# Performance work log

Hardware: AMD Instinct MI355X
Metric: run time of the kernel (lower is better)

The kernel has to match this reference:

```python
import jax, jax.numpy as jnp
import numpy as np

SOS_TOKEN = 0
EOS_TOKEN = 29
B, S, ENC = 128, 400, 512   # batch, encoder max seq len, encoder feature dim
E, H, D, P, V = 256, 512, 128, 128, 30  # embed, dec hidden, dec out, attn proj, vocab
T = 600  # inference timesteps


def setup_inputs() -> dict:
    key = jax.random.key(0)
    ks = jax.random.split(key, 20)
    u = lambda k, sh: jax.random.uniform(k, sh, jnp.float32, -0.1, 0.1)
    n = lambda k, sh, s=0.02: s * jax.random.normal(k, sh, jnp.float32)
    embed = n(ks[0], (V, E), 1.0).at[EOS_TOKEN].set(0.0)  # padding_idx=EOS
    inp = dict(
        encoder_outputs=jax.random.normal(ks[1], (B, S, ENC), jnp.float32),
        encoder_lens=jax.random.randint(ks[2], (B,), S // 2, S + 1),
        embed=embed,
        W_ih1=u(ks[3], (4 * H, E + P)), W_hh1=u(ks[4], (4 * H, H)),
        b_ih1=u(ks[5], (4 * H,)), b_hh1=u(ks[6], (4 * H,)),
        W_ih2=u(ks[7], (4 * D, H)), W_hh2=u(ks[8], (4 * D, D)),
        b_ih2=u(ks[9], (4 * D,)), b_hh2=u(ks[10], (4 * D,)),
        Wk=n(ks[11], (P, ENC)), bk=jnp.zeros((P,), jnp.float32),
        Wv=n(ks[12], (P, ENC)), bv=jnp.zeros((P,), jnp.float32),
        Wq=n(ks[13], (P, D)), bq=jnp.zeros((P,), jnp.float32),
        b_char=jnp.zeros((V,), jnp.float32),
    )
    return inp


def _lstm_cell(x, h, c, W_ih, W_hh, b_ih, b_hh):
    gates = x @ W_ih.T + h @ W_hh.T + b_ih + b_hh
    i, f, g, o = jnp.split(gates, 4, axis=-1)
    c2 = jax.nn.sigmoid(f) * c + jax.nn.sigmoid(i) * jnp.tanh(g)
    return jax.nn.sigmoid(o) * jnp.tanh(c2), c2


def reference(encoder_outputs, encoder_lens, embed,
              W_ih1, W_hh1, b_ih1, b_hh1,
              W_ih2, W_hh2, b_ih2, b_hh2,
              Wk, bk, Wv, bv, Wq, bq, b_char):
    # precompute attention keys/values and mask (set_key_value_mask)
    keyv = encoder_outputs @ Wk.T + bk           # [B, S, P]
    valv = encoder_outputs @ Wv.T + bv           # [B, S, P]
    mask = jnp.arange(S)[None, :] < encoder_lens[:, None]  # [B, S]
    scale = 1.0 / np.sqrt(P).astype(np.float32)

    char0 = jnp.full((B,), SOS_TOKEN, jnp.int32)
    h1 = jnp.zeros((B, H), jnp.float32); c1 = jnp.zeros((B, H), jnp.float32)
    h2 = jnp.zeros((B, D), jnp.float32); c2 = jnp.zeros((B, D), jnp.float32)
    ctx0 = jnp.zeros((B, P), jnp.float32)

    def step(carry, _):
        char, h1, c1, h2, c2, ctx = carry
        ce = embed[char]                                   # [B, E]
        x = jnp.concatenate([ce, ctx], axis=1)
        h1n, c1n = _lstm_cell(x, h1, c1, W_ih1, W_hh1, b_ih1, b_hh1)
        h2n, c2n = _lstm_cell(h1n, h2, c2, W_ih2, W_hh2, b_ih2, b_hh2)
        q = h2n @ Wq.T + bq                                # [B, P] (attention.query)
        e = jnp.einsum('bsp,bp->bs', keyv, q) * scale
        w = jax.nn.softmax(jnp.where(mask, e, -1e9), axis=-1)
        ctxn = jnp.einsum('bs,bsp->bp', w, valv)           # [B, P]
        out_emb = jnp.concatenate([q, ctxn], axis=1)       # [B, P+P] == [B, E]
        pred = out_emb @ embed.T + b_char                  # tied char_prob weight
        charn = jnp.argmax(pred, axis=1).astype(jnp.int32)
        return (charn, h1n, c1n, h2n, c2n, ctxn), (pred, w[0])

    _, (preds, attn0) = jax.lax.scan(step, (char0, h1, c1, h2, c2, ctx0), None, length=T)
    predictions = jnp.transpose(preds, (1, 0, 2))  # [B, T, V]
    attention_plot = attn0                          # [T, S]
    return predictions, attention_plot
```

## Files before the change

kernel.cpp:

```cpp
#include <hip/hip_runtime.h>
#include <math.h>

#define B_   128
#define S_   400
#define ENC_ 512
#define E_   256
#define H_   512
#define D_   128
#define P_   128
#define V_   30
#define T_   600

#define KEYV_OFF 0
#define VALV_OFF (KEYV_OFF + B_*S_*P_)
#define H1_OFF   (VALV_OFF + B_*S_*P_)
#define H2T_OFF  (H1_OFF + 2*H_*B_)
#define H2R_OFF  (H2T_OFF + 2*D_*B_)
#define CTXT_OFF (H2R_OFF + B_*D_)
#define CHR_OFF  (CTXT_OFF + P_*B_)
#define WS_FLOATS (CHR_OFF + B_)

#define PRED_N (B_*T_*V_)
#define NBLK 256
#define NTHR 512

#define W1_BASE 0
#define W2_BASE 14336
#define SCR     24576
#define LDS_FLOATS (SCR + 13120)

__device__ __forceinline__ float sigm_(float x){ return 1.0f/(1.0f + expf(-x)); }

__device__ __forceinline__ float ldA(const float* p){
  return __hip_atomic_load(p, __ATOMIC_RELAXED, __HIP_MEMORY_SCOPE_AGENT);
}
__device__ __forceinline__ void stA(float* p, float v){
  __hip_atomic_store(p, v, __ATOMIC_RELAXED, __HIP_MEMORY_SCOPE_AGENT);
}
__device__ __forceinline__ int ldAi(const int* p){
  return __hip_atomic_load(p, __ATOMIC_RELAXED, __HIP_MEMORY_SCOPE_AGENT);
}
__device__ __forceinline__ void stAi(int* p, int v){
  __hip_atomic_store(p, v, __ATOMIC_RELAXED, __HIP_MEMORY_SCOPE_AGENT);
}
__device__ __forceinline__ void ldA2f(const float* p, float& a, float& b){
  unsigned long long v = __hip_atomic_load((const unsigned long long*)p,
                         __ATOMIC_RELAXED, __HIP_MEMORY_SCOPE_AGENT);
  a = __uint_as_float((unsigned)v);
  b = __uint_as_float((unsigned)(v>>32));
}

__device__ __forceinline__ void gbar(int* bar){
  asm volatile("s_waitcnt vmcnt(0)" ::: "memory");
  __syncthreads();
  if (threadIdx.x == 0){
    const int g0 = __hip_atomic_load(bar, __ATOMIC_RELAXED, __HIP_MEMORY_SCOPE_AGENT);
    asm volatile("" ::: "memory");
    int* leaf = bar + 64 + (blockIdx.x & 7)*32;
    int lo = __hip_atomic_fetch_add(leaf, 1, __ATOMIC_RELAXED, __HIP_MEMORY_SCOPE_AGENT);
    bool done = false;
    if (lo == 31){
      int ro = __hip_atomic_fetch_add(bar+32, 1, __ATOMIC_RELAXED, __HIP_MEMORY_SCOPE_AGENT);
      if (ro == 7){
        #pragma unroll
        for (int i=0;i<8;++i)
          __hip_atomic_store(bar+64+i*32, 0, __ATOMIC_RELAXED, __HIP_MEMORY_SCOPE_AGENT);
        __hip_atomic_store(bar+32, 0, __ATOMIC_RELAXED, __HIP_MEMORY_SCOPE_AGENT);
        asm volatile("s_waitcnt vmcnt(0)" ::: "memory");
        __hip_atomic_fetch_add(bar, 1, __ATOMIC_RELAXED, __HIP_MEMORY_SCOPE_AGENT);
        done = true;
      }
    }
    if (!done){
      while (__hip_atomic_load(bar, __ATOMIC_RELAXED, __HIP_MEMORY_SCOPE_AGENT) == g0)
        __builtin_amdgcn_s_sleep(4);
    }
  }
  __syncthreads();
}

__global__ __launch_bounds__(256) void k_kv(const float* __restrict__ enc,
    const float* __restrict__ Wk, const float* __restrict__ bk,
    const float* __restrict__ Wv, const float* __restrict__ bv,
    float* __restrict__ ws)
{
  __shared__ float As[32][68];
  __shared__ float Bs[32][68];
  const int tid = threadIdx.x;
  const int tx = tid & 15, ty = tid >> 4;
  const int n0 = blockIdx.x * 64;
  const int c0 = blockIdx.y * 64;
  float acc[4][4] = {};
  for (int k0 = 0; k0 < ENC_; k0 += 32){
    #pragma unroll
    for (int i = 0; i < 8; ++i){
      int idx = tid + 256*i;
      int kk = idx & 31, nl = idx >> 5;
      As[kk][nl] = enc[(size_t)(n0+nl)*ENC_ + k0 + kk];
    }
    #pragma unroll
    for (int i = 0; i < 8; ++i){
      int idx = tid + 256*i;
      int kk = idx & 31, cl = idx >> 5;
      int c = c0 + cl; int p = c & 127;
      const float* W = (c < 128) ? Wk : Wv;
      Bs[kk][cl] = W[(size_t)p*ENC_ + k0 + kk];
    }
    __syncthreads();
    #pragma unroll
    for (int kk = 0; kk < 32; ++kk){
      float4 a4 = *(const float4*)&As[kk][ty*4];
      float4 b4 = *(const float4*)&Bs[kk][tx*4];
      float aa[4] = {a4.x, a4.y, a4.z, a4.w};
      float bb[4] = {b4.x, b4.y, b4.z, b4.w};
      #pragma unroll
      for (int i=0;i<4;++i)
        #pragma unroll
        for (int j=0;j<4;++j) acc[i][j] += aa[i]*bb[j];
    }
    __syncthreads();
  }
  float* keyv = ws + KEYV_OFF;
  float* valv = ws + VALV_OFF;
  #pragma unroll
  for (int i=0;i<4;++i){
    int n = n0 + ty*4 + i; int b = n / S_; int s = n - b*S_;
    #pragma unroll
    for (int j=0;j<4;++j){
      int c = c0 + tx*4 + j;
      float v = acc[i][j];
      if (c < 128) keyv[((size_t)b*S_+s)*P_ + c]       = v + bk[c];
      else         valv[((size_t)b*S_+s)*P_ + (c-128)] = v + bv[c-128];
    }
  }
}

__global__ __launch_bounds__(NTHR, 1) void k_persist(
    const float* __restrict__ embed,
    const float* __restrict__ Wih1, const float* __restrict__ Whh1,
    const float* __restrict__ bih1, const float* __restrict__ bhh1,
    const float* __restrict__ Wih2, const float* __restrict__ Whh2,
    const float* __restrict__ bih2, const float* __restrict__ bhh2,
    const float* __restrict__ Wq, const float* __restrict__ bq,
    const float* __restrict__ bchar, const int* __restrict__ lens,
    float* ws, float* out)
{
  extern __shared__ float smem[];
  const int tid = threadIdx.x;
  const int bid = blockIdx.x;
  int* bar = (int*)(ws + WS_FLOATS);

  float* ctxT = ws + CTXT_OFF;
  int*   chrg = (int*)(ws + CHR_OFF);
  float* h2R  = ws + H2R_OFF;

  float* Wl  = smem + W1_BASE;
  float* W2l = smem + W2_BASE;
  float* scr = smem + SCR;

  const int lane = tid & 63;
  const int so8  = tid >> 6;

  const int ib = bid & 1, ug = bid >> 1, b0 = ib*64;
  const int iq = lane & 15, rq = lane >> 4;
  const int u1 = tid >> 6;
  const int J1 = ug*4 + (u1 & 3);
  const int sA  = (tid & 31)*2;
  const int kbA = tid >> 5;

  const int ig2 = bid & 3, ug2 = bid >> 2, b02 = ig2*32;
  const int iq2 = lane & 7, rq2 = lane >> 3;
  const int u2 = tid >> 5;
  const int J2 = ug2*4 + (u2 & 3);
  const int sB  = (tid & 15)*2;
  const int kbB = tid >> 4;

  const int it3 = bid & 127;
  const float* keyv3 = ws + KEYV_OFF + (size_t)it3*S_*P_;
  const float* valv3 = ws + VALV_OFF + (size_t)it3*S_*P_;
  const int lenb = lens[it3];
  const float bqr  = bq[tid >> 2];
  const float bchr = ((tid >> 4) < V_) ? bchar[tid >> 4] : 0.f;
  float* qs3   = scr;
  float* es3   = scr + 128;
  float* hs3   = scr + 528;
  float* redw3 = scr + 656;
  float* red33 = scr + 672;
  float* oes3  = scr + 2784;
  float* pred3 = scr + 3040;

  {
    const int r = tid & 15, kb = tid >> 4;
    const int R = (r >> 2)*H_ + ug*4 + (r & 3);
    for (int j = 0; j < 28; ++j){
      int k = kb*28 + j;
      float v = (k < 384) ? Wih1[(size_t)R*384 + k] : Whh1[(size_t)R*H_ + (k-384)];
      Wl[k*16 + r] = v;
    }
  }
  if (bid < 128){
    const int r = tid & 15, kb = tid >> 4;
    const int R = (r >> 2)*D_ + ug2*4 + (r & 3);
    for (int j = 0; j < 20; ++j){
      int k = kb*20 + j;
      float v = (k < 512) ? Wih2[(size_t)R*H_ + k] : Whh2[(size_t)R*D_ + (k-512)];
      W2l[k*16 + r] = v;
    }
  }
  __syncthreads();

  float c1r = 0.f, c2r = 0.f;
  float b1s[4], b2s[4];
  #pragma unroll
  for (int g=0; g<4; ++g){
    b1s[g] = bih1[g*H_ + J1] + bhh1[g*H_ + J1];
    b2s[g] = (bid < 128) ? (bih2[g*D_ + J2] + bhh2[g*D_ + J2]) : 0.f;
  }

  for (int t = 0; t < T_; ++t){
    {
      const float* h1oT = ws + H1_OFF + (size_t)(t&1)*H_*B_;
      float*       h1nT = ws + H1_OFF + (size_t)((t+1)&1)*H_*B_;
      float* Xs  = scr;
      float* red = scr + 4096;
      int*   schs= (int*)(scr + 12800);

      if (tid < 64) schs[tid] = ldAi(chrg + b0 + tid);
      __syncthreads();
      const int chA = schs[sA], chB = schs[sA+1];

      float xr[4][8];
      auto LOADX = [&](int p, float* dst){
        if (p < 4){
          const float4 va = *(const float4*)(embed + (size_t)chA*E_ + p*64 + kbA*4);
          const float4 vb = *(const float4*)(embed + (size_t)chB*E_ + p*64 + kbA*4);
          dst[0]=va.x; dst[1]=vb.x; dst[2]=va.y; dst[3]=vb.y;
          dst[4]=va.z; dst[5]=vb.z; dst[6]=va.w; dst[7]=vb.w;
        } else {
          const float* base = (p < 6) ? (ctxT + (size_t)(p*64-256)*B_)
                                      : (h1oT + (size_t)(p*64-384)*B_);
          #pragma unroll
          for (int j=0;j<4;++j)
            ldA2f(base + (size_t)(kbA*4+j)*B_ + b0 + sA, dst[j*2], dst[j*2+1]);
        }
      };
      LOADX(0,xr[0]); LOADX(1,xr[1]); LOADX(2,xr[2]); LOADX(3,xr[3]);

      float acc[4][4] = {};
      for (int p = 0; p < 14; ++p){
        float* xc = xr[p&3];
        #pragma unroll
        for (int j=0;j<4;++j){
          const int kl = kbA*4 + j;
          *(float2*)&Xs[kl*64 + (((sA>>2)+kl)&15)*4 + (sA&3)]
            = make_float2(xc[j*2], xc[j*2+1]);
        }
        __syncthreads();
        if (p + 4 < 14) LOADX(p + 4, xr[p&3]);
        float4 xv[8], wv[8];
        #pragma unroll
        for (int it = 0; it < 8; ++it){
          const int kl = so8*8 + it;
          xv[it] = *(const float4*)&Xs[kl*64 + ((iq + kl)&15)*4];
          wv[it] = *(const float4*)&Wl[(p*64 + kl)*16 + rq*4];
        }
        #pragma unroll
        for (int it = 0; it < 8; ++it){
          float xa[4] = {xv[it].x, xv[it].y, xv[it].z, xv[it].w};
          float wa[4] = {wv[it].x, wv[it].y, wv[it].z, wv[it].w};
          #pragma unroll
          for (int i=0;i<4;++i)
            #pragma unroll
            for (int j=0;j<4;++j) acc[i][j] += xa[i]*wa[j];
        }
        __syncthreads();
      }
      #pragma unroll
      for (int j=0;j<4;++j)
        *(float4*)&red[so8*1088 + (rq*4+j)*68 + iq*4]
          = make_float4(acc[0][j], acc[1][j], acc[2][j], acc[3][j]);
      __syncthreads();
      if (tid < 256){
        const int item = tid & 63;
        float gate[4];
        #pragma unroll
        for (int g=0; g<4; ++g){
          float s = 0.f;
          #pragma unroll
          for (int w=0; w<8; ++w) s += red[w*1088 + (g*4+(u1&3))*68 + item];
          gate[g] = s + b1s[g];
        }
        float cn = sigm_(gate[1])*c1r + sigm_(gate[0])*tanhf(gate[2]);
        float hn = sigm_(gate[3])*tanhf(cn);
        c1r = cn;
        stA(h1nT + (size_t)J1*B_ + b0 + item, hn);
      }
    }
    gbar(bar);

    if (bid < 128){
      const float* h1nT = ws + H1_OFF + (size_t)((t+1)&1)*H_*B_;
      const float* h2oT = ws + H2T_OFF + (size_t)(t&1)*D_*B_;
      float*       h2nT = ws + H2T_OFF + (size_t)((t+1)&1)*D_*B_;
      float* Xs2  = scr;
      float* red2 = scr + 2048;

      float xr2[4][4];
      auto LOADX2 = [&](int p, float* dst){
        const float* base = (p < 8) ? (h1nT + (size_t)(p*64)*B_)
                                    : (h2oT + (size_t)(p*64-512)*B_);
        #pragma unroll
        for (int j=0;j<2;++j)
          ldA2f(base + (size_t)(kbB*2+j)*B_ + b02 + sB, dst[j*2], dst[j*2+1]);
      };
      LOADX2(0,xr2[0]); LOADX2(1,xr2[1]); LOADX2(2,xr2[2]); LOADX2(3,xr2[3]);

      float acc2[4][2] = {};
      for (int p = 0; p < 10; ++p){
        float* xc = xr2[p&3];
        #pragma unroll
        for (int j=0;j<2;++j){
          const int kl = kbB*2 + j;
          *(float2*)&Xs2[kl*32 + (((sB>>2)+kl)&7)*4 + (sB&3)]
            = make_float2(xc[j*2], xc[j*2+1]);
        }
        __syncthreads();
        if (p + 4 < 10) LOADX2(p + 4, xr2[p&3]);
        float4 xv2[8]; float2 wv2[8];
        #pragma unroll
        for (int it = 0; it < 8; ++it){
          const int kl = so8*8 + it;
          xv2[it] = *(const float4*)&Xs2[kl*32 + ((iq2 + kl)&7)*4];
          wv2[it] = *(const float2*)&W2l[(p*64 + kl)*16 + rq2*2];
        }
        #pragma unroll
        for (int it = 0; it < 8; ++it){
          float xa[4] = {xv2[it].x, xv2[it].y, xv2[it].z, xv2[it].w};
          #pragma unroll
          for (int i=0;i<4;++i){
            acc2[i][0] += xa[i]*wv2[it].x;
            acc2[i][1] += xa[i]*wv2[it].y;
          }
        }
        __syncthreads();
      }
      #pragma unroll
      for (int j=0;j<2;++j)
        *(float4*)&red2[so8*576 + (rq2*2+j)*36 + iq2*4]
          = make_float4(acc2[0][j], acc2[1][j], acc2[2][j], acc2[3][j]);
      __syncthreads();
      if (tid < 128){
        const int item = tid & 31;
        float gate[4];
        #pragma unroll
        for (int g=0; g<4; ++g){
          float s = 0.f;
          #pragma unroll
          for (int w=0; w<8; ++w) s += red2[w*576 + (g*4+(u2&3))*36 + item];
          gate[g] = s + b2s[g];
        }
        float cn = sigm_(gate[1])*c2r + sigm_(gate[0])*tanhf(gate[2]);
        float hn = sigm_(gate[3])*tanhf(cn);
        c2r = cn;
        stA(h2nT + (size_t)J2*B_ + b02 + item, hn);
        stA(h2R  + (size_t)(b02+item)*D_ + J2, hn);
      }
    } else {
      float wacc = 0.f;
      const float4* kp = (const float4*)keyv3;
      #pragma unroll
      for (int j = 0; j < 8; ++j){
        float4 v = kp[tid + j*512];
        wacc += v.x + v.y + v.z + v.w;
      }
      asm volatile("" :: "v"(wacc));
    }
    gbar(bar);

    if (bid >= 128){
      if (tid < 128) hs3[tid] = ldA(h2R + (size_t)it3*D_ + tid);
      __syncthreads();
      {
        const int r = tid >> 2, kq = tid & 3;
        const float* wr = Wq + (size_t)r*D_ + kq*32;
        float a = 0.f;
        #pragma unroll
        for (int j=0;j<8;++j){
          float4 wvq = *(const float4*)(wr + j*4);
          float4 hv = *(const float4*)&hs3[kq*32 + j*4];
          a += wvq.x*hv.x + wvq.y*hv.y + wvq.z*hv.z + wvq.w*hv.w;
        }
        a += __shfl_down(a, 2, 4);
        a += __shfl_down(a, 1, 4);
        if (kq == 0) qs3[r] = a + bqr;
      }
      __syncthreads();
      float sv = -INFINITY;
      if (tid < lenb){
        const float4* kr = (const float4*)(keyv3 + (size_t)tid*P_);
        float a = 0.f;
        #pragma unroll 8
        for (int d=0; d<32; ++d){
          float4 kv = kr[d];
          float4 qv = *(const float4*)&qs3[d*4];
          a += kv.x*qv.x + kv.y*qv.y + kv.z*qv.z + kv.w*qv.w;
        }
        sv = a * 0.08838834764831845f;
      }
      float mv = sv;
      #pragma unroll
      for (int o=32; o; o>>=1) mv = fmaxf(mv, __shfl_xor(mv, o));
      if ((tid & 63) == 0) redw3[tid >> 6] = mv;
      __syncthreads();
      const float m = fmaxf(fmaxf(fmaxf(redw3[0],redw3[1]),fmaxf(redw3[2],redw3[3])),
                            fmaxf(fmaxf(redw3[4],redw3[5]),fmaxf(redw3[6],redw3[7])));
      float pv = 0.f;
      if (tid < lenb){ pv = expf(sv - m); es3[tid] = pv; }
      float sm = pv;
      #pragma unroll
      for (int o=32; o; o>>=1) sm += __shfl_xor(sm, o);
      if ((tid & 63) == 0) redw3[8 + (tid >> 6)] = sm;
      __syncthreads();
      const float sum = ((redw3[8]+redw3[9])+(redw3[10]+redw3[11]))
                      + ((redw3[12]+redw3[13])+(redw3[14]+redw3[15]));
      {
        const int p4 = tid & 31, sg = tid >> 5;
        float a0=0,a1=0,a2=0,a3=0;
        const int rend = min(sg*25 + 25, lenb);
        #pragma unroll 4
        for (int r = sg*25; r < rend; ++r){
          float e = es3[r];
          float4 v = *(const float4*)(valv3 + (size_t)r*P_ + p4*4);
          a0 += e*v.x; a1 += e*v.y; a2 += e*v.z; a3 += e*v.w;
        }
        *(float4*)&red33[sg*132 + p4*4] = make_float4(a0,a1,a2,a3);
      }
      __syncthreads();
      if (tid < 128){
        float c = 0.f;
        #pragma unroll
        for (int sg=0; sg<16; ++sg) c += red33[sg*132 + tid];
        c /= sum;
        stA(ctxT + (size_t)tid*B_ + it3, c);
        oes3[tid] = qs3[tid]; oes3[128+tid] = c;
      }
      __syncthreads();
      {
        const int v = tid >> 4, k16 = tid & 15;
        float a = 0.f;
        if (v < V_){
          const float4* er = (const float4*)(embed + (size_t)v*E_ + k16*16);
          #pragma unroll
          for (int j=0;j<4;++j){
            float4 ev = er[j];
            float4 ov = *(const float4*)&oes3[k16*16 + j*4];
            a += ev.x*ov.x + ev.y*ov.y + ev.z*ov.z + ev.w*ov.w;
          }
        }
        a += __shfl_down(a, 8, 16);
        a += __shfl_down(a, 4, 16);
        a += __shfl_down(a, 2, 16);
        a += __shfl_down(a, 1, 16);
        if (v < V_ && k16 == 0){
          float pvv = a + bchr;
          pred3[v] = pvv;
          out[((size_t)it3*T_ + t)*V_ + v] = pvv;
        }
      }
      __syncthreads();
      if (tid < 32){
        float val = (tid < V_) ? pred3[tid] : -INFINITY;
        int idx = tid;
        #pragma unroll
        for (int o = 16; o > 0; o >>= 1){
          float ov = __shfl_down(val, o, 32);
          int oi = __shfl_down(idx, o, 32);
          if (ov > val || (ov == val && oi < idx)){ val = ov; idx = oi; }
        }
        if (tid == 0) stAi(chrg + it3, idx);
      }
      if (it3 == 0 && tid < S_)
        out[PRED_N + (size_t)t*S_ + tid] = (tid < lenb) ? es3[tid]/sum : 0.f;
    }
    gbar(bar);
  }
}

extern "C" void kernel_launch(void* const* d_in, const int* in_sizes, int n_in,
                              void* d_out, int out_size, void* d_ws, size_t ws_size,
                              hipStream_t stream)
{
  (void)in_sizes; (void)n_in; (void)out_size; (void)ws_size;
  const float* enc   = (const float*)d_in[0];
  const int*   lens  = (const int*)d_in[1];
  const float* embed = (const float*)d_in[2];
  const float* Wih1  = (const float*)d_in[3];
  const float* Whh1  = (const float*)d_in[4];
  const float* bih1  = (const float*)d_in[5];
  const float* bhh1  = (const float*)d_in[6];
  const float* Wih2  = (const float*)d_in[7];
  const float* Whh2  = (const float*)d_in[8];
  const float* bih2  = (const float*)d_in[9];
  const float* bhh2  = (const float*)d_in[10];
  const float* Wk    = (const float*)d_in[11];
  const float* bk    = (const float*)d_in[12];
  const float* Wv    = (const float*)d_in[13];
  const float* bv    = (const float*)d_in[14];
  const float* Wq    = (const float*)d_in[15];
  const float* bq    = (const float*)d_in[16];
  const float* bchar = (const float*)d_in[17];
  float* out = (float*)d_out;
  float* ws  = (float*)d_ws;

  hipMemsetAsync((char*)d_ws + (size_t)H1_OFF*sizeof(float), 0,
                 (size_t)(WS_FLOATS - H1_OFF)*sizeof(float) + 2048, stream);
  hipLaunchKernelGGL(k_kv, dim3(800,4), dim3(256), 0, stream, enc, Wk, bk, Wv, bv, ws);

  hipFuncSetAttribute((const void*)k_persist,
                      hipFuncAttributeMaxDynamicSharedMemorySize, LDS_FLOATS*4);
  hipLaunchKernelGGL(k_persist, dim3(NBLK), dim3(NTHR), LDS_FLOATS*4, stream,
                     embed, Wih1, Whh1, bih1, bhh1,
                     Wih2, Whh2, bih2, bhh2,
                     Wq, bq, bchar, lens, ws, out);
}
```

Before: 25.77 ms.

## Split attention across two blocks per batch row and defer combine into next step

The attention phase now runs on all 256 blocks: each batch row's sequence is split into two halves of up to 200 positions. Each half computes partial max, sum and weighted values, and the second block merges them with a log-sum-exp combine. The combine, projection and argmax are deferred into the start of the next timestep. The LSTM1 matmul is reordered so the h1 panels are computed first, and a counter spin-wait holds off the embedding and context panels until the combine has published the new chars and context. This doubles attention parallelism and overlaps the output head with LSTM1 work, at the cost of extra workspace traffic and an extra fine-grained sync.

Result: slower. 61.84 ms (+139.9%).

```diff
diff --git a/kernel.cpp b/kernel.cpp
--- a/kernel.cpp
+++ b/kernel.cpp
@@ -18,7 +18,10 @@
 #define H2R_OFF  (H2T_OFF + 2*D_*B_)
 #define CTXT_OFF (H2R_OFF + B_*D_)
 #define CHR_OFF  (CTXT_OFF + P_*B_)
-#define WS_FLOATS (CHR_OFF + B_)
+#define PV0_OFF  (CHR_OFF + B_)
+#define MS0_OFF  (PV0_OFF + B_*P_)
+#define ES0_OFF  (MS0_OFF + 2*B_)
+#define WS_FLOATS (ES0_OFF + 200)
 
 #define PRED_N (B_*T_*V_)
 #define NBLK 256
@@ -27,7 +30,7 @@
 #define W1_BASE 0
 #define W2_BASE 14336
 #define SCR     24576
-#define LDS_FLOATS (SCR + 13120)
+#define LDS_FLOATS (SCR + 13312)
 
 __device__ __forceinline__ float sigm_(float x){ return 1.0f/(1.0f + expf(-x)); }
 
@@ -148,15 +151,22 @@
   extern __shared__ float smem[];
   const int tid = threadIdx.x;
   const int bid = blockIdx.x;
-  int* bar = (int*)(ws + WS_FLOATS);
+  int* bar  = (int*)(ws + WS_FLOATS);
+  int* cnt2 = bar + 512;
 
   float* ctxT = ws + CTXT_OFF;
   int*   chrg = (int*)(ws + CHR_OFF);
   float* h2R  = ws + H2R_OFF;
+  float* pv0g = ws + PV0_OFF;
+  float* ms0g = ws + MS0_OFF;
+  float* es0g = ws + ES0_OFF;
 
   float* Wl  = smem + W1_BASE;
   float* W2l = smem + W2_BASE;
   float* scr = smem + SCR;
+  float* qs3k   = scr + 12864;
+  float* oesA   = scr + 12992;
+  float* pred3A = scr + 13248;
 
   const int lane = tid & 63;
   const int so8  = tid >> 6;
@@ -175,19 +185,15 @@
   const int sB  = (tid & 15)*2;
   const int kbB = tid >> 4;
 
+  const int h3  = bid >> 7;
   const int it3 = bid & 127;
   const float* keyv3 = ws + KEYV_OFF + (size_t)it3*S_*P_;
   const float* valv3 = ws + VALV_OFF + (size_t)it3*S_*P_;
   const int lenb = lens[it3];
+  const int cw  = h3 ? (lenb - 200) : 200;
+  const int s0w = h3*200;
   const float bqr  = bq[tid >> 2];
   const float bchr = ((tid >> 4) < V_) ? bchar[tid >> 4] : 0.f;
-  float* qs3   = scr;
-  float* es3   = scr + 128;
-  float* hs3   = scr + 528;
-  float* redw3 = scr + 656;
-  float* red33 = scr + 672;
-  float* oes3  = scr + 2784;
-  float* pred3 = scr + 3040;
 
   {
     const int r = tid & 15, kb = tid >> 4;
@@ -217,6 +223,59 @@
     b2s[g] = (bid < 128) ? (bih2[g*D_ + J2] + bhh2[g*D_ + J2]) : 0.f;
   }
 
+  float mhK = -INFINITY, smK = 0.f, pvcK = 0.f, esK = 0.f;
+
+  auto COMBINE = [&](int tp){
+    const float m0 = ldA(ms0g + it3*2), s0v = ldA(ms0g + it3*2 + 1);
+    const float m  = fmaxf(m0, mhK);
+    const float e0 = expf(m0 - m), e1 = expf(mhK - m);
+    const float sum = s0v*e0 + smK*e1;
+    if (tid < 128){
+      float c = (ldA(pv0g + (size_t)it3*P_ + tid)*e0 + pvcK*e1) / sum;
+      stA(ctxT + (size_t)tid*B_ + it3, c);
+      oesA[tid] = qs3k[tid]; oesA[128+tid] = c;
+    }
+    __syncthreads();
+    {
+      const int v = tid >> 4, k16 = tid & 15;
+      float a = 0.f;
+      if (v < V_){
+        const float4* er = (const float4*)(embed + (size_t)v*E_ + k16*16);
+        #pragma unroll
+        for (int j=0;j<4;++j){
+          float4 ev = er[j];
+          float4 ov = *(const float4*)&oesA[k16*16 + j*4];
+          a += ev.x*ov.x + ev.y*ov.y + ev.z*ov.z + ev.w*ov.w;
+        }
+      }
+      a += __shfl_down(a, 8, 16);
+      a += __shfl_down(a, 4, 16);
+      a += __shfl_down(a, 2, 16);
+      a += __shfl_down(a, 1, 16);
+      if (v < V_ && k16 == 0){
+        float pvv = a + bchr;
+        pred3A[v] = pvv;
+        out[((size_t)it3*T_ + tp)*V_ + v] = pvv;
+      }
+    }
+    __syncthreads();
+    if (tid < 32){
+      float val = (tid < V_) ? pred3A[tid] : -INFINITY;
+      int idx = tid;
+      #pragma unroll
+      for (int o = 16; o > 0; o >>= 1){
+        float ov = __shfl_down(val, o, 32);
+        int oi = __shfl_down(idx, o, 32);
+        if (ov > val || (ov == val && oi < idx)){ val = ov; idx = oi; }
+      }
+      if (tid == 0) stAi(chrg + it3, idx);
+    }
+    if (it3 == 0 && tid < S_){
+      float v = (tid < 200) ? ldA(es0g + tid)*e0 : esK*e1;
+      out[PRED_N + (size_t)tp*S_ + tid] = v / sum;
+    }
+  };
+
   for (int t = 0; t < T_; ++t){
     {
       const float* h1oT = ws + H1_OFF + (size_t)(t&1)*H_*B_;
@@ -225,38 +284,36 @@
       float* red = scr + 4096;
       int*   schs= (int*)(scr + 12800);
 
-      if (tid < 64) schs[tid] = ldAi(chrg + b0 + tid);
-      __syncthreads();
-      const int chA = schs[sA], chB = schs[sA+1];
+      if (bid >= 128 && t > 0){
+        COMBINE(t-1);
+        asm volatile("s_waitcnt vmcnt(0)" ::: "memory");
+        __syncthreads();
+        if (tid == 0)
+          (void)__hip_atomic_fetch_add(cnt2, 1, __ATOMIC_RELAXED, __HIP_MEMORY_SCOPE_AGENT);
+      }
 
       float xr[4][8];
-      auto LOADX = [&](int p, float* dst){
-        if (p < 4){
-          const float4 va = *(const float4*)(embed + (size_t)chA*E_ + p*64 + kbA*4);
-          const float4 vb = *(const float4*)(embed + (size_t)chB*E_ + p*64 + kbA*4);
-          dst[0]=va.x; dst[1]=vb.x; dst[2]=va.y; dst[3]=vb.y;
-          dst[4]=va.z; dst[5]=vb.z; dst[6]=va.w; dst[7]=vb.w;
-        } else {
-          const float* base = (p < 6) ? (ctxT + (size_t)(p*64-256)*B_)
-                                      : (h1oT + (size_t)(p*64-384)*B_);
-          #pragma unroll
-          for (int j=0;j<4;++j)
-            ldA2f(base + (size_t)(kbA*4+j)*B_ + b0 + sA, dst[j*2], dst[j*2+1]);
-        }
+      float acc[4][4] = {};
+      int chA = 0, chB = 0;
+      auto LOADH = [&](int p, float* dst){
+        const float* base = h1oT + (size_t)(p*64-384)*B_;
+        #pragma unroll
+        for (int j=0;j<4;++j)
+          ldA2f(base + (size_t)(kbA*4+j)*B_ + b0 + sA, dst[j*2], dst[j*2+1]);
       };
-      LOADX(0,xr[0]); LOADX(1,xr[1]); LOADX(2,xr[2]); LOADX(3,xr[3]);
-
-      float acc[4][4] = {};
-      for (int p = 0; p < 14; ++p){
-        float* xc = xr[p&3];
-        #pragma unroll
-        for (int j=0;j<4;++j){
-          const int kl = kbA*4 + j;
-          *(float2*)&Xs[kl*64 + (((sA>>2)+kl)&15)*4 + (sA&3)]
-            = make_float2(xc[j*2], xc[j*2+1]);
-        }
-        __syncthreads();
-        if (p + 4 < 14) LOADX(p + 4, xr[p&3]);
+      auto LOADE = [&](int p, float* dst){
+        const float4 va = *(const float4*)(embed + (size_t)chA*E_ + p*64 + kbA*4);
+        const float4 vb = *(const float4*)(embed + (size_t)chB*E_ + p*64 + kbA*4);
+        dst[0]=va.x; dst[1]=vb.x; dst[2]=va.y; dst[3]=vb.y;
+        dst[4]=va.z; dst[5]=vb.z; dst[6]=va.w; dst[7]=vb.w;
+      };
+      auto LOADC = [&](int p, float* dst){
+        const float* base = ctxT + (size_t)(p*64-256)*B_;
+        #pragma unroll
+        for (int j=0;j<4;++j)
+          ldA2f(base + (size_t)(kbA*4+j)*B_ + b0 + sA, dst[j*2], dst[j*2+1]);
+      };
+      auto PANEL = [&](int p){
         float4 xv[8], wv[8];
         #pragma unroll
         for (int it = 0; it < 8; ++it){
@@ -273,6 +330,40 @@
             #pragma unroll
             for (int j=0;j<4;++j) acc[i][j] += xa[i]*wa[j];
         }
+      };
+      auto STORE = [&](float* xc){
+        #pragma unroll
+        for (int j=0;j<4;++j){
+          const int kl = kbA*4 + j;
+          *(float2*)&Xs[kl*64 + (((sA>>2)+kl)&15)*4 + (sA&3)]
+            = make_float2(xc[j*2], xc[j*2+1]);
+        }
+      };
+
+      LOADH(6, xr[0]); LOADH(7, xr[1]); LOADH(8, xr[2]); LOADH(9, xr[3]);
+      for (int s = 0; s < 8; ++s){
+        STORE(xr[s & 3]);
+        __syncthreads();
+        if (s < 4) LOADH(s + 10, xr[s & 3]);
+        PANEL(s + 6);
+        __syncthreads();
+      }
+      if (tid == 0){
+        while (ldAi(cnt2) < 128*t) __builtin_amdgcn_s_sleep(1);
+      }
+      __syncthreads();
+      if (tid < 64) schs[tid] = ldAi(chrg + b0 + tid);
+      __syncthreads();
+      chA = schs[sA]; chB = schs[sA+1];
+      LOADE(0, xr[0]); LOADE(1, xr[1]);
+      for (int s = 0; s < 6; ++s){
+        STORE(xr[s & 1]);
+        __syncthreads();
+        if (s + 2 < 6){
+          if (s + 2 < 4) LOADE(s + 2, xr[s & 1]);
+          else           LOADC(s + 2, xr[s & 1]);
+        }
+        PANEL(s);
         __syncthreads();
       }
       #pragma unroll
@@ -365,19 +456,15 @@
         stA(h2nT + (size_t)J2*B_ + b02 + item, hn);
         stA(h2R  + (size_t)(b02+item)*D_ + J2, hn);
       }
-    } else {
-      float wacc = 0.f;
-      const float4* kp = (const float4*)keyv3;
-      #pragma unroll
-      for (int j = 0; j < 8; ++j){
-        float4 v = kp[tid + j*512];
-        wacc += v.x + v.y + v.z + v.w;
-      }
-      asm volatile("" :: "v"(wacc));
     }
     gbar(bar);
 
-    if (bid >= 128){
+    {
+      float* es3  = scr;
+      float* hs3  = scr + 208;
+      float* redw = scr + 336;
+      float* red33= scr + 352;
+      if (tid < 208) es3[tid] = 0.f;
       if (tid < 128) hs3[tid] = ldA(h2R + (size_t)it3*D_ + tid);
       __syncthreads();
       {
@@ -392,97 +479,76 @@
         }
         a += __shfl_down(a, 2, 4);
         a += __shfl_down(a, 1, 4);
-        if (kq == 0) qs3[r] = a + bqr;
-      }
-      __syncthreads();
+        if (kq == 0) qs3k[r] = a + bqr;
+      }
+      __syncthreads();
+      const int r2 = tid >> 1, hseg = tid & 1;
       float sv = -INFINITY;
-      if (tid < lenb){
-        const float4* kr = (const float4*)(keyv3 + (size_t)tid*P_);
+      if (r2 < cw){
+        const float4* kr = (const float4*)(keyv3 + (size_t)(s0w + r2)*P_ + hseg*64);
         float a = 0.f;
         #pragma unroll 8
-        for (int d=0; d<32; ++d){
+        for (int d=0; d<16; ++d){
           float4 kv = kr[d];
-          float4 qv = *(const float4*)&qs3[d*4];
+          float4 qv = *(const float4*)&qs3k[hseg*64 + d*4];
           a += kv.x*qv.x + kv.y*qv.y + kv.z*qv.z + kv.w*qv.w;
         }
-        sv = a * 0.08838834764831845f;
+        a += __shfl_down(a, 1, 2);
+        if (hseg == 0) sv = a * 0.08838834764831845f;
       }
       float mv = sv;
       #pragma unroll
       for (int o=32; o; o>>=1) mv = fmaxf(mv, __shfl_xor(mv, o));
-      if ((tid & 63) == 0) redw3[tid >> 6] = mv;
-      __syncthreads();
-      const float m = fmaxf(fmaxf(fmaxf(redw3[0],redw3[1]),fmaxf(redw3[2],redw3[3])),
-                            fmaxf(fmaxf(redw3[4],redw3[5]),fmaxf(redw3[6],redw3[7])));
-      float pv = 0.f;
-      if (tid < lenb){ pv = expf(sv - m); es3[tid] = pv; }
-      float sm = pv;
+      if ((tid & 63) == 0) redw[tid >> 6] = mv;
+      __syncthreads();
+      const float mh = fmaxf(fmaxf(fmaxf(redw[0],redw[1]),fmaxf(redw[2],redw[3])),
+                             fmaxf(fmaxf(redw[4],redw[5]),fmaxf(redw[6],redw[7])));
+      float pvx = 0.f;
+      if (r2 < cw && hseg == 0){ pvx = expf(sv - mh); es3[r2] = pvx; }
+      float sm = pvx;
       #pragma unroll
       for (int o=32; o; o>>=1) sm += __shfl_xor(sm, o);
-      if ((tid & 63) == 0) redw3[8 + (tid >> 6)] = sm;
-      __syncthreads();
-      const float sum = ((redw3[8]+redw3[9])+(redw3[10]+redw3[11]))
-                      + ((redw3[12]+redw3[13])+(redw3[14]+redw3[15]));
+      if ((tid & 63) == 0) redw[8 + (tid >> 6)] = sm;
+      __syncthreads();
+      const float sumh = ((redw[8]+redw[9])+(redw[10]+redw[11]))
+                       + ((redw[12]+redw[13])+(redw[14]+redw[15]));
       {
         const int p4 = tid & 31, sg = tid >> 5;
         float a0=0,a1=0,a2=0,a3=0;
-        const int rend = min(sg*25 + 25, lenb);
-        #pragma unroll 4
-        for (int r = sg*25; r < rend; ++r){
+        const int rbeg = sg*13, rend = min(rbeg + 13, cw);
+        for (int r = rbeg; r < rend; ++r){
           float e = es3[r];
-          float4 v = *(const float4*)(valv3 + (size_t)r*P_ + p4*4);
+          float4 v = *(const float4*)(valv3 + (size_t)(s0w + r)*P_ + p4*4);
           a0 += e*v.x; a1 += e*v.y; a2 += e*v.z; a3 += e*v.w;
         }
         *(float4*)&red33[sg*132 + p4*4] = make_float4(a0,a1,a2,a3);
       }
       __syncthreads();
-      if (tid < 128){
-        float c = 0.f;
-        #pragma unroll
-        for (int sg=0; sg<16; ++sg) c += red33[sg*132 + tid];
-        c /= sum;
-        stA(ctxT + (size_t)tid*B_ + it3, c);
-        oes3[tid] = qs3[tid]; oes3[128+tid] = c;
-      }
-      __syncthreads();
-      {
-        const int v = tid >> 4, k16 = tid & 15;
-        float a = 0.f;
-        if (v < V_){
-          const float4* er = (const float4*)(embed + (size_t)v*E_ + k16*16);
+      if (h3 == 0){
+        if (tid < 128){
+          float c = 0.f;
           #pragma unroll
-          for (int j=0;j<4;++j){
-            float4 ev = er[j];
-            float4 ov = *(const float4*)&oes3[k16*16 + j*4];
-            a += ev.x*ov.x + ev.y*ov.y + ev.z*ov.z + ev.w*ov.w;
-          }
-        }
-        a += __shfl_down(a, 8, 16);
-        a += __shfl_down(a, 4, 16);
-        a += __shfl_down(a, 2, 16);
-        a += __shfl_down(a, 1, 16);
-        if (v < V_ && k16 == 0){
-          float pvv = a + bchr;
-          pred3[v] = pvv;
-          out[((size_t)it3*T_ + t)*V_ + v] = pvv;
-        }
-      }
-      __syncthreads();
-      if (tid < 32){
-        float val = (tid < V_) ? pred3[tid] : -INFINITY;
-        int idx = tid;
-        #pragma unroll
-        for (int o = 16; o > 0; o >>= 1){
-          float ov = __shfl_down(val, o, 32);
-          int oi = __shfl_down(idx, o, 32);
-          if (ov > val || (ov == val && oi < idx)){ val = ov; idx = oi; }
-        }
-        if (tid == 0) stAi(chrg + it3, idx);
-      }
-      if (it3 == 0 && tid < S_)
-        out[PRED_N + (size_t)t*S_ + tid] = (tid < lenb) ? es3[tid]/sum : 0.f;
+          for (int sg=0; sg<16; ++sg) c += red33[sg*132 + tid];
+          stA(pv0g + (size_t)it3*P_ + tid, c);
+        }
+        if (tid == 0){ stA(ms0g + it3*2, mh); stA(ms0g + it3*2 + 1, sumh); }
+        if (it3 == 0 && tid < 200) stA(es0g + tid, es3[tid]);
+      } else {
+        if (tid < 128){
+          float c = 0.f;
+          #pragma unroll
+          for (int sg=0; sg<16; ++sg) c += red33[sg*132 + tid];
+          pvcK = c;
+        }
+        mhK = mh; smK = sumh;
+        if (tid >= 200 && tid < 400) esK = es3[tid - 200];
+      }
     }
     gbar(bar);
+  }
+
+  if (bid >= 128){
+    COMBINE(T_ - 1);
   }
 }
 
@@ -513,7 +579,7 @@
   float* ws  = (float*)d_ws;
 
   hipMemsetAsync((char*)d_ws + (size_t)H1_OFF*sizeof(float), 0,
-                 (size_t)(WS_FLOATS - H1_OFF)*sizeof(float) + 2048, stream);
+                 (size_t)(WS_FLOATS - H1_OFF)*sizeof(float) + 4096, stream);
   hipLaunchKernelGGL(k_kv, dim3(800,4), dim3(256), 0, stream, enc, Wk, bk, Wv, bv, ws);
 
   hipFuncSetAttribute((const void*)k_persist,
```

## Double block size to 1024 threads and repartition all three phases

Applied to the files above, without the earlier changes.

Raises threads per block from 512 to 1024 and re-splits the work in every phase of the persistent kernel. Each thread now computes a 2x4 tile instead of 4x4 in LSTM1, half the K range in LSTM2, and half a key row in the attention scores, with more partial sums reduced afterwards. The change also drops the dummy keyv warm-read loop in the idle blocks. It trades fewer serial iterations per thread for more LDS reduction traffic, more threads taking part in each __syncthreads, and possibly register-limited occupancy at 1024 threads.

Measured after the change: 31.33 ms. 21.6% more time.

```diff
diff --git a/kernel.cpp b/kernel.cpp
--- a/kernel.cpp
+++ b/kernel.cpp
@@ -22,7 +22,7 @@
 
 #define PRED_N (B_*T_*V_)
 #define NBLK 256
-#define NTHR 512
+#define NTHR 1024
 
 #define W1_BASE 0
 #define W2_BASE 14336
@@ -159,10 +159,13 @@
   float* scr = smem + SCR;
 
   const int lane = tid & 63;
-  const int so8  = tid >> 6;
+  const int so16 = tid >> 6;
 
   const int ib = bid & 1, ug = bid >> 1, b0 = ib*64;
-  const int iq = lane & 15, rq = lane >> 4;
+  const int w8 = so16 & 7;
+  const int g1 = so16 >> 3;
+  const int ip = lane & 15;
+  const int rq = lane >> 4;
   const int u1 = tid >> 6;
   const int J1 = ug*4 + (u1 & 3);
   const int sA  = (tid & 31)*2;
@@ -179,21 +182,22 @@
   const float* keyv3 = ws + KEYV_OFF + (size_t)it3*S_*P_;
   const float* valv3 = ws + VALV_OFF + (size_t)it3*S_*P_;
   const int lenb = lens[it3];
-  const float bqr  = bq[tid >> 2];
+  const float bqr  = bq[tid >> 3];
   const float bchr = ((tid >> 4) < V_) ? bchar[tid >> 4] : 0.f;
-  float* qs3   = scr;
-  float* es3   = scr + 128;
-  float* hs3   = scr + 528;
-  float* redw3 = scr + 656;
-  float* red33 = scr + 672;
-  float* oes3  = scr + 2784;
-  float* pred3 = scr + 3040;
+  float* es3   = scr;
+  float* hs3   = scr + 408;
+  float* qs3   = scr + 536;
+  float* redw3 = scr + 664;
+  float* red33 = scr + 696;
+  float* oes3  = scr + 4920;
+  float* pred3 = scr + 5176;
 
   {
     const int r = tid & 15, kb = tid >> 4;
     const int R = (r >> 2)*H_ + ug*4 + (r & 3);
-    for (int j = 0; j < 28; ++j){
-      int k = kb*28 + j;
+    #pragma unroll
+    for (int j = 0; j < 14; ++j){
+      int k = kb*14 + j;
       float v = (k < 384) ? Wih1[(size_t)R*384 + k] : Whh1[(size_t)R*H_ + (k-384)];
       Wl[k*16 + r] = v;
     }
@@ -201,8 +205,9 @@
   if (bid < 128){
     const int r = tid & 15, kb = tid >> 4;
     const int R = (r >> 2)*D_ + ug2*4 + (r & 3);
-    for (int j = 0; j < 20; ++j){
-      int k = kb*20 + j;
+    #pragma unroll
+    for (int j = 0; j < 10; ++j){
+      int k = kb*10 + j;
       float v = (k < 512) ? Wih2[(size_t)R*H_ + k] : Whh2[(size_t)R*D_ + (k-512)];
       W2l[k*16 + r] = v;
     }
@@ -229,56 +234,60 @@
       __syncthreads();
       const int chA = schs[sA], chB = schs[sA+1];
 
-      float xr[4][8];
+      float xr[4][4];
       auto LOADX = [&](int p, float* dst){
         if (p < 4){
-          const float4 va = *(const float4*)(embed + (size_t)chA*E_ + p*64 + kbA*4);
-          const float4 vb = *(const float4*)(embed + (size_t)chB*E_ + p*64 + kbA*4);
-          dst[0]=va.x; dst[1]=vb.x; dst[2]=va.y; dst[3]=vb.y;
-          dst[4]=va.z; dst[5]=vb.z; dst[6]=va.w; dst[7]=vb.w;
+          #pragma unroll
+          for (int j=0;j<2;++j){
+            int kg = p*64 + kbA*2 + j;
+            dst[j*2]   = embed[(size_t)chA*E_ + kg];
+            dst[j*2+1] = embed[(size_t)chB*E_ + kg];
+          }
         } else {
           const float* base = (p < 6) ? (ctxT + (size_t)(p*64-256)*B_)
                                       : (h1oT + (size_t)(p*64-384)*B_);
           #pragma unroll
-          for (int j=0;j<4;++j)
-            ldA2f(base + (size_t)(kbA*4+j)*B_ + b0 + sA, dst[j*2], dst[j*2+1]);
+          for (int j=0;j<2;++j)
+            ldA2f(base + (size_t)(kbA*2+j)*B_ + b0 + sA, dst[j*2], dst[j*2+1]);
         }
       };
       LOADX(0,xr[0]); LOADX(1,xr[1]); LOADX(2,xr[2]); LOADX(3,xr[3]);
 
-      float acc[4][4] = {};
+      float acc[2][4] = {};
+      #pragma unroll
       for (int p = 0; p < 14; ++p){
         float* xc = xr[p&3];
         #pragma unroll
-        for (int j=0;j<4;++j){
-          const int kl = kbA*4 + j;
+        for (int j=0;j<2;++j){
+          const int kl = kbA*2 + j;
           *(float2*)&Xs[kl*64 + (((sA>>2)+kl)&15)*4 + (sA&3)]
             = make_float2(xc[j*2], xc[j*2+1]);
         }
         __syncthreads();
         if (p + 4 < 14) LOADX(p + 4, xr[p&3]);
-        float4 xv[8], wv[8];
+        float2 xv[8]; float4 wv[8];
         #pragma unroll
         for (int it = 0; it < 8; ++it){
-          const int kl = so8*8 + it;
-          xv[it] = *(const float4*)&Xs[kl*64 + ((iq + kl)&15)*4];
+          const int kl = w8*8 + it;
+          const int s4 = (g1*8 + (ip>>1) + kl) & 15;
+          xv[it] = *(const float2*)&Xs[kl*64 + s4*4 + (ip&1)*2];
           wv[it] = *(const float4*)&Wl[(p*64 + kl)*16 + rq*4];
         }
         #pragma unroll
         for (int it = 0; it < 8; ++it){
-          float xa[4] = {xv[it].x, xv[it].y, xv[it].z, xv[it].w};
           float wa[4] = {wv[it].x, wv[it].y, wv[it].z, wv[it].w};
           #pragma unroll
-          for (int i=0;i<4;++i)
-            #pragma unroll
-            for (int j=0;j<4;++j) acc[i][j] += xa[i]*wa[j];
+          for (int j=0;j<4;++j){
+            acc[0][j] += xv[it].x*wa[j];
+            acc[1][j] += xv[it].y*wa[j];
+          }
         }
         __syncthreads();
       }
       #pragma unroll
       for (int j=0;j<4;++j)
-        *(float4*)&red[so8*1088 + (rq*4+j)*68 + iq*4]
-          = make_float4(acc[0][j], acc[1][j], acc[2][j], acc[3][j]);
+        *(float2*)&red[w8*1088 + (rq*4+j)*68 + g1*32 + ip*2]
+          = make_float2(acc[0][j], acc[1][j]);
       __syncthreads();
       if (tid < 256){
         const int item = tid & 63;
@@ -305,36 +314,31 @@
       float* Xs2  = scr;
       float* red2 = scr + 2048;
 
-      float xr2[4][4];
+      float xr2[4][2];
       auto LOADX2 = [&](int p, float* dst){
         const float* base = (p < 8) ? (h1nT + (size_t)(p*64)*B_)
                                     : (h2oT + (size_t)(p*64-512)*B_);
-        #pragma unroll
-        for (int j=0;j<2;++j)
-          ldA2f(base + (size_t)(kbB*2+j)*B_ + b02 + sB, dst[j*2], dst[j*2+1]);
+        ldA2f(base + (size_t)kbB*B_ + b02 + sB, dst[0], dst[1]);
       };
       LOADX2(0,xr2[0]); LOADX2(1,xr2[1]); LOADX2(2,xr2[2]); LOADX2(3,xr2[3]);
 
       float acc2[4][2] = {};
+      #pragma unroll
       for (int p = 0; p < 10; ++p){
         float* xc = xr2[p&3];
-        #pragma unroll
-        for (int j=0;j<2;++j){
-          const int kl = kbB*2 + j;
-          *(float2*)&Xs2[kl*32 + (((sB>>2)+kl)&7)*4 + (sB&3)]
-            = make_float2(xc[j*2], xc[j*2+1]);
-        }
+        *(float2*)&Xs2[kbB*32 + (((sB>>2)+kbB)&7)*4 + (sB&3)]
+          = make_float2(xc[0], xc[1]);
         __syncthreads();
         if (p + 4 < 10) LOADX2(p + 4, xr2[p&3]);
-        float4 xv2[8]; float2 wv2[8];
-        #pragma unroll
-        for (int it = 0; it < 8; ++it){
-          const int kl = so8*8 + it;
+        float4 xv2[4]; float2 wv2[4];
+        #pragma unroll
+        for (int it = 0; it < 4; ++it){
+          const int kl = so16*4 + it;
           xv2[it] = *(const float4*)&Xs2[kl*32 + ((iq2 + kl)&7)*4];
           wv2[it] = *(const float2*)&W2l[(p*64 + kl)*16 + rq2*2];
         }
         #pragma unroll
-        for (int it = 0; it < 8; ++it){
+        for (int it = 0; it < 4; ++it){
           float xa[4] = {xv2[it].x, xv2[it].y, xv2[it].z, xv2[it].w};
           #pragma unroll
           for (int i=0;i<4;++i){
@@ -346,7 +350,7 @@
       }
       #pragma unroll
       for (int j=0;j<2;++j)
-        *(float4*)&red2[so8*576 + (rq2*2+j)*36 + iq2*4]
+        *(float4*)&red2[so16*576 + (rq2*2+j)*36 + iq2*4]
           = make_float4(acc2[0][j], acc2[1][j], acc2[2][j], acc2[3][j]);
       __syncthreads();
       if (tid < 128){
@@ -356,7 +360,7 @@
         for (int g=0; g<4; ++g){
           float s = 0.f;
           #pragma unroll
-          for (int w=0; w<8; ++w) s += red2[w*576 + (g*4+(u2&3))*36 + item];
+          for (int w=0; w<16; ++w) s += red2[w*576 + (g*4+(u2&3))*36 + item];
           gate[g] = s + b2s[g];
         }
         float cn = sigm_(gate[1])*c2r + sigm_(gate[0])*tanhf(gate[2]);
@@ -365,70 +369,66 @@
         stA(h2nT + (size_t)J2*B_ + b02 + item, hn);
         stA(h2R  + (size_t)(b02+item)*D_ + J2, hn);
       }
-    } else {
-      float wacc = 0.f;
-      const float4* kp = (const float4*)keyv3;
-      #pragma unroll
-      for (int j = 0; j < 8; ++j){
-        float4 v = kp[tid + j*512];
-        wacc += v.x + v.y + v.z + v.w;
-      }
-      asm volatile("" :: "v"(wacc));
     }
     gbar(bar);
 
     if (bid >= 128){
+      if (tid < 408) es3[tid] = 0.f;
       if (tid < 128) hs3[tid] = ldA(h2R + (size_t)it3*D_ + tid);
       __syncthreads();
       {
-        const int r = tid >> 2, kq = tid & 3;
-        const float* wr = Wq + (size_t)r*D_ + kq*32;
+        const int r = tid >> 3, kq = tid & 7;
+        const float* wr = Wq + (size_t)r*D_ + kq*16;
         float a = 0.f;
         #pragma unroll
-        for (int j=0;j<8;++j){
+        for (int j=0;j<4;++j){
           float4 wvq = *(const float4*)(wr + j*4);
-          float4 hv = *(const float4*)&hs3[kq*32 + j*4];
+          float4 hv = *(const float4*)&hs3[kq*16 + j*4];
           a += wvq.x*hv.x + wvq.y*hv.y + wvq.z*hv.z + wvq.w*hv.w;
         }
-        a += __shfl_down(a, 2, 4);
-        a += __shfl_down(a, 1, 4);
+        a += __shfl_down(a, 4, 8);
+        a += __shfl_down(a, 2, 8);
+        a += __shfl_down(a, 1, 8);
         if (kq == 0) qs3[r] = a + bqr;
       }
       __syncthreads();
+      const int r2 = tid >> 1, hseg = tid & 1;
       float sv = -INFINITY;
-      if (tid < lenb){
-        const float4* kr = (const float4*)(keyv3 + (size_t)tid*P_);
+      if (r2 < lenb){
+        const float4* kr = (const float4*)(keyv3 + (size_t)r2*P_ + hseg*64);
         float a = 0.f;
         #pragma unroll 8
-        for (int d=0; d<32; ++d){
+        for (int d=0; d<16; ++d){
           float4 kv = kr[d];
-          float4 qv = *(const float4*)&qs3[d*4];
+          float4 qv = *(const float4*)&qs3[hseg*64 + d*4];
           a += kv.x*qv.x + kv.y*qv.y + kv.z*qv.z + kv.w*qv.w;
         }
-        sv = a * 0.08838834764831845f;
+        a += __shfl_down(a, 1, 2);
+        if (hseg == 0) sv = a * 0.08838834764831845f;
       }
       float mv = sv;
       #pragma unroll
       for (int o=32; o; o>>=1) mv = fmaxf(mv, __shfl_xor(mv, o));
       if ((tid & 63) == 0) redw3[tid >> 6] = mv;
       __syncthreads();
-      const float m = fmaxf(fmaxf(fmaxf(redw3[0],redw3[1]),fmaxf(redw3[2],redw3[3])),
-                            fmaxf(fmaxf(redw3[4],redw3[5]),fmaxf(redw3[6],redw3[7])));
+      float m = redw3[0];
+      #pragma unroll
+      for (int w=1; w<16; ++w) m = fmaxf(m, redw3[w]);
       float pv = 0.f;
-      if (tid < lenb){ pv = expf(sv - m); es3[tid] = pv; }
+      if (r2 < lenb && hseg == 0){ pv = expf(sv - m); es3[r2] = pv; }
       float sm = pv;
       #pragma unroll
       for (int o=32; o; o>>=1) sm += __shfl_xor(sm, o);
-      if ((tid & 63) == 0) redw3[8 + (tid >> 6)] = sm;
-      __syncthreads();
-      const float sum = ((redw3[8]+redw3[9])+(redw3[10]+redw3[11]))
-                      + ((redw3[12]+redw3[13])+(redw3[14]+redw3[15]));
+      if ((tid & 63) == 0) redw3[16 + (tid >> 6)] = sm;
+      __syncthreads();
+      float sum = 0.f;
+      #pragma unroll
+      for (int w=0; w<16; ++w) sum += redw3[16+w];
       {
         const int p4 = tid & 31, sg = tid >> 5;
         float a0=0,a1=0,a2=0,a3=0;
-        const int rend = min(sg*25 + 25, lenb);
-        #pragma unroll 4
-        for (int r = sg*25; r < rend; ++r){
+        const int rend = min(sg*13 + 13, lenb);
+        for (int r = sg*13; r < rend; ++r){
           float e = es3[r];
           float4 v = *(const float4*)(valv3 + (size_t)r*P_ + p4*4);
           a0 += e*v.x; a1 += e*v.y; a2 += e*v.z; a3 += e*v.w;
@@ -439,7 +439,7 @@
       if (tid < 128){
         float c = 0.f;
         #pragma unroll
-        for (int sg=0; sg<16; ++sg) c += red33[sg*132 + tid];
+        for (int sg=0; sg<32; ++sg) c += red33[sg*132 + tid];
         c /= sum;
         stA(ctxT + (size_t)tid*B_ + it3, c);
         oes3[tid] = qs3[tid]; oes3[128+tid] = c;
```
